# Performance work log

Hardware: AMD Instinct MI355X
Metric: run time of the kernel (lower is better)

Reference implementation:

```python
import jax, jax.numpy as jnp
import numpy as np

B, S, H, R = 32, 1024, 768, 24
ATT_EPS = 1e10
LN_EPS = 1e-12


def setup_inputs() -> dict:
    key = jax.random.key(0)
    ks = jax.random.split(key, 20)
    sc = 0.02
    inp = {
        "relation": jax.random.randint(ks[0], (B, 1), 0, R),
        "last_hidden_size": jax.random.normal(ks[1], (B, S, H), dtype=jnp.float32),
        "sub_head": jax.random.randint(ks[2], (B, 1), 0, S),
        "sub_tail": jax.random.randint(ks[3], (B, 1), 0, S),
        "attention_mask": jnp.ones((B, S), dtype=jnp.float32),
        # learned parameters
        "rel_emb": jax.random.normal(ks[4], (R, H)) * sc,
        "W_rf": jax.random.normal(ks[5], (H, H)) * sc,
        "b_rf": jnp.zeros((H,), jnp.float32),
        "gamma": jnp.ones((H,), jnp.float32),
        "beta": jnp.zeros((H,), jnp.float32),
        "W_wd": jax.random.normal(ks[6], (H, 2 * H)) * sc,
        "W_bd": jax.random.normal(ks[7], (H, 2 * H)) * sc,
        "Wq": jax.random.normal(ks[8], (H, H)) * sc,
        "bq": jnp.zeros((H,), jnp.float32),
        "Wk": jax.random.normal(ks[9], (H, H)) * sc,
        "bk": jnp.zeros((H,), jnp.float32),
        "Wv": jax.random.normal(ks[10], (H, H)) * sc,
        "bv": jnp.zeros((H,), jnp.float32),
        "W_obj": jax.random.normal(ks[11], (1, H)) * sc,
        "b_obj": jnp.zeros((1,), jnp.float32),
    }
    return inp


def reference(relation, last_hidden_size, sub_head, sub_tail, attention_mask,
              rel_emb, W_rf, b_rf, gamma, beta, W_wd, W_bd,
              Wq, bq, Wk, bk, Wv, bv, W_obj, b_obj):
    # dropout layers are identity in eval mode
    # relation feature: embedding -> linear -> ReLU6   [B,1,H]
    rel_feature = jnp.clip(rel_emb[relation] @ W_rf.T + b_rf, 0.0, 6.0)
    # subject span features via gather                 [B,1,H]
    sh = jnp.take_along_axis(last_hidden_size, sub_head[:, :, None], axis=1)
    st = jnp.take_along_axis(last_hidden_size, sub_tail[:, :, None], axis=1)
    sub_feature = (sh + st) * 0.5
    cond = jnp.concatenate([rel_feature, sub_feature], axis=-1)  # [B,1,2H]

    # conditional layer norm: per-sample affine from condition
    weight = cond @ W_wd.T + gamma  # [B,1,H]
    bias = cond @ W_bd.T + beta     # [B,1,H]
    mean = jnp.mean(last_hidden_size, axis=-1, keepdims=True)
    ctr = last_hidden_size - mean
    var = jnp.mean(ctr * ctr, axis=-1, keepdims=True)
    x = ctr / jnp.sqrt(var + LN_EPS)
    x = x * weight + bias  # [B,S,H]

    # custom attention: ReLU-activated q/k/v, additive mask bias, residual
    q = jax.nn.relu(x @ Wq.T + bq)
    k = jax.nn.relu(x @ Wk.T + bk)
    v = jax.nn.relu(x @ Wv.T + bv)
    e = jnp.einsum('bsh,bth->bst', q, k)  # [B,S,S]
    e = e - ATT_EPS * (1.0 - attention_mask[:, None, :])
    a = jax.nn.softmax(e, axis=-1)
    hidden = jnp.einsum('bst,bth->bsh', a, v) + x  # residual

    pred_obj_head = jnp.squeeze(hidden @ W_obj.T + b_obj, axis=-1)  # [B,S]
    return pred_obj_head, hidden
```

## Files before the change

kernel.cpp:

```cpp
#include <hip/hip_runtime.h>

constexpr int NB  = 32;
constexpr int NS  = 1024;
constexpr int NH  = 768;
constexpr int NH2 = 1536;
constexpr int NQKV = 2304;
constexpr int NBS = NB * NS;

typedef __bf16 bf16x8 __attribute__((ext_vector_type(8)));
typedef float  f32x4  __attribute__((ext_vector_type(4)));
typedef unsigned short u16x8 __attribute__((ext_vector_type(8)));

__device__ __forceinline__ unsigned short f2bf(float f) {
  unsigned int u = __builtin_bit_cast(unsigned int, f);
  u += 0x7FFFu + ((u >> 16) & 1u);
  return (unsigned short)(u >> 16);
}
__device__ __forceinline__ float bf2f(unsigned short h) {
  return __builtin_bit_cast(float, ((unsigned int)h) << 16);
}

#define GLDS16(g, l)                                                         \
  __builtin_amdgcn_global_load_lds(                                          \
      (__attribute__((address_space(1))) void*)(g),                          \
      (__attribute__((address_space(3))) void*)(l), 16, 0, 0)

__launch_bounds__(256)
__global__ void cond_pre(const int* __restrict__ relation,
                         const float* __restrict__ h,
                         const int* __restrict__ subh,
                         const int* __restrict__ subt,
                         const float* __restrict__ rel_emb,
                         float* __restrict__ reT, float* __restrict__ condT) {
  const int b = blockIdx.x, t = threadIdx.x;
  const int r = relation[b], sh = subh[b], st = subt[b];
  for (int k = t; k < NH; k += 256) {
    reT[(size_t)k * NB + b] = rel_emb[(size_t)r * NH + k];
    condT[(size_t)(NH + k) * NB + b] =
        0.5f * (h[((size_t)b * NS + sh) * NH + k] +
                h[((size_t)b * NS + st) * NH + k]);
  }
}

__launch_bounds__(256)
__global__ void cond_rf(const float* __restrict__ W_rf,
                        const float* __restrict__ b_rf,
                        const float* __restrict__ reT,
                        float* __restrict__ condT) {
  const int t = threadIdx.x;
  const int b = t & 31, jl = t >> 5;
  const int j = blockIdx.x * 8 + jl;
  const float4* w4 = (const float4*)(W_rf + (size_t)j * NH);
  const float* rT = reT + b;
  float a0 = 0.f, a1 = 0.f;
  for (int k4 = 0; k4 < NH / 4; k4++) {
    float4 w = w4[k4];
    const float* c = rT + (size_t)(k4 * 4) * NB;
    a0 += w.x * c[0] + w.y * c[NB];
    a1 += w.z * c[2 * NB] + w.w * c[3 * NB];
  }
  float acc = a0 + a1 + b_rf[j];
  condT[(size_t)j * NB + b] = fminf(fmaxf(acc, 0.0f), 6.0f);
}

__launch_bounds__(256)
__global__ void cond_wb(const float* __restrict__ W_wd,
                        const float* __restrict__ W_bd,
                        const float* __restrict__ gamma,
                        const float* __restrict__ beta,
                        const float* __restrict__ condT,
                        float* __restrict__ wt, float* __restrict__ bs) {
  __shared__ float redW[128], redB[128];
  const int t = threadIdx.x;
  const int b = t & 31, jl = (t >> 5) & 3, ks = t >> 7;
  const int j = blockIdx.x * 4 + jl;
  const float4* ww = (const float4*)(W_wd + (size_t)j * NH2 + ks * NH);
  const float4* wb = (const float4*)(W_bd + (size_t)j * NH2 + ks * NH);
  const float* cT = condT + (size_t)ks * NH * NB + b;
  float aw0 = 0.f, aw1 = 0.f, ab0 = 0.f, ab1 = 0.f;
  for (int k4 = 0; k4 < NH / 4; k4++) {
    float4 w = ww[k4];
    float4 v = wb[k4];
    const float* c = cT + (size_t)(k4 * 4) * NB;
    float c0 = c[0], c1 = c[NB], c2 = c[2 * NB], c3 = c[3 * NB];
    aw0 += w.x * c0 + w.y * c1;
    aw1 += w.z * c2 + w.w * c3;
    ab0 += v.x * c0 + v.y * c1;
    ab1 += v.z * c2 + v.w * c3;
  }
  float aw = aw0 + aw1, ab = ab0 + ab1;
  if (ks == 1) {
    redW[t - 128] = aw;
    redB[t - 128] = ab;
  }
  __syncthreads();
  if (ks == 0) {
    aw += redW[t];
    ab += redB[t];
    wt[(size_t)b * NH + j] = aw + gamma[j];
    bs[(size_t)b * NH + j] = ab + beta[j];
  }
}

__launch_bounds__(64)
__global__ void ln_kernel(const float* __restrict__ h,
                          const float* __restrict__ wt,
                          const float* __restrict__ bs,
                          unsigned short* __restrict__ xbf) {
  const int row = blockIdx.x;
  const int b = row >> 10;
  const int lane = threadIdx.x;
  const float4* hr = (const float4*)(h + (size_t)row * NH);
  float4 v0 = hr[lane], v1 = hr[lane + 64], v2 = hr[lane + 128];
  float sum = 0.f, sq = 0.f;
  {
    sum += v0.x + v0.y + v0.z + v0.w;
    sq  += v0.x * v0.x + v0.y * v0.y + v0.z * v0.z + v0.w * v0.w;
    sum += v1.x + v1.y + v1.z + v1.w;
    sq  += v1.x * v1.x + v1.y * v1.y + v1.z * v1.z + v1.w * v1.w;
    sum += v2.x + v2.y + v2.z + v2.w;
    sq  += v2.x * v2.x + v2.y * v2.y + v2.z * v2.z + v2.w * v2.w;
  }
  for (int off = 32; off > 0; off >>= 1) {
    sum += __shfl_xor(sum, off, 64);
    sq  += __shfl_xor(sq, off, 64);
  }
  const float mean = sum * (1.0f / NH);
  const float var  = sq * (1.0f / NH) - mean * mean;
  const float rstd = rsqrtf(var + 1e-12f);
  const float4* wr = (const float4*)(wt + (size_t)b * NH);
  const float4* br = (const float4*)(bs + (size_t)b * NH);
  ushort4* xr = (ushort4*)(xbf + (size_t)row * NH);
#pragma unroll
  for (int i = 0; i < 3; i++) {
    float4 v = (i == 0) ? v0 : (i == 1) ? v1 : v2;
    float4 w = wr[lane + 64 * i];
    float4 bb = br[lane + 64 * i];
    ushort4 o;
    o.x = f2bf((v.x - mean) * rstd * w.x + bb.x);
    o.y = f2bf((v.y - mean) * rstd * w.y + bb.y);
    o.z = f2bf((v.z - mean) * rstd * w.z + bb.z);
    o.w = f2bf((v.w - mean) * rstd * w.w + bb.w);
    xr[lane + 64 * i] = o;
  }
}

__launch_bounds__(256)
__global__ void prep_w(const float* __restrict__ Wq, const float* __restrict__ bq,
                       const float* __restrict__ Wk, const float* __restrict__ bk,
                       const float* __restrict__ Wv, const float* __restrict__ bv,
                       unsigned short* __restrict__ Wcat, float* __restrict__ bcat) {
  const int row = blockIdx.x;
  const float* Wsrc;
  const float* bsrc;
  int r;
  if (row < NH) { Wsrc = Wq; bsrc = bq; r = row; }
  else if (row < NH2) { Wsrc = Wk; bsrc = bk; r = row - NH; }
  else { Wsrc = Wv; bsrc = bv; r = row - NH2; }
  for (int j = threadIdx.x; j < NH; j += 256)
    Wcat[(size_t)row * NH + j] = f2bf(Wsrc[(size_t)r * NH + j]);
  if (threadIdx.x == 0) bcat[row] = bsrc[r];
}

template <int OUT_BF16, int RELU, int HASBIAS, int RES>
__launch_bounds__(256, 4)
__global__ void gemm128(const unsigned short* __restrict__ A, long long sAz, int lda,
                        const unsigned short* __restrict__ Bm, long long sBz, int ldb,
                        void* __restrict__ C, long long sCz, int ldc,
                        const float* __restrict__ bias,
                        const unsigned short* __restrict__ Res, long long sRz, int ldr,
                        int K) {
  __shared__ char lds[32768];
  const int t = threadIdx.x;
  const int gx = gridDim.x, gxy = gridDim.x * gridDim.y;
  int n = blockIdx.x + gridDim.x * (blockIdx.y + gridDim.y * blockIdx.z);
  int wid;
  {
    const int nwg = gxy * gridDim.z;
    const int q = nwg >> 3, r = nwg & 7;
    const int xcd = n & 7, lid = n >> 3;
    wid = (xcd < r ? xcd * (q + 1) : r * (q + 1) + (xcd - r) * q) + lid;
  }
  const int z = wid / gxy;
  const int rem = wid % gxy;
  const int tileN = (rem % gx) * 128;
  const int tileM = (rem / gx) * 128;
  const unsigned short* Ab = A + (size_t)z * sAz + (size_t)tileM * lda;
  const unsigned short* Bb = Bm + (size_t)z * sBz + (size_t)tileN * ldb;

  const int lane = t & 63;
  const int w = t >> 6;
  const int wm = w >> 1, wn = w & 1;
  const int lr = lane & 15, hi = lane >> 4;
  const int cbyte = ((hi ^ ((lr >> 1) & 3)) << 4);

  const int sgc = (t & 3) ^ ((t >> 3) & 3);

#define STAGEOP(Gb, ld, kc, dst)                                            \
  do {                                                                      \
    GLDS16((Gb) + (size_t)(t >> 2) * (ld) + (kc) + sgc * 8,                 \
           (dst) + (size_t)t * 16);                                         \
    GLDS16((Gb) + (size_t)(64 + (t >> 2)) * (ld) + (kc) + sgc * 8,          \
           (dst) + 4096 + (size_t)t * 16);                                  \
  } while (0)

  f32x4 acc[4][4];
#pragma unroll
  for (int m = 0; m < 4; m++)
#pragma unroll
    for (int n2 = 0; n2 < 4; n2++) acc[m][n2] = (f32x4)0.0f;

  const int NT = K >> 5;

  STAGEOP(Ab, lda, 0, lds);
  STAGEOP(Bb, ldb, 0, lds + 8192);
  __syncthreads();

  for (int kt = 0; kt < NT; kt++) {
    const int bb = kt & 1;
    const char* Ah = lds + bb * 16384;
    const char* Bh = Ah + 8192;
    if (kt + 1 < NT) {
      STAGEOP(Ab, lda, (kt + 1) * 32, lds + (bb ^ 1) * 16384);
      STAGEOP(Bb, ldb, (kt + 1) * 32, lds + (bb ^ 1) * 16384 + 8192);
    }
    bf16x8 aF[4], bF[4];
#pragma unroll
    for (int i = 0; i < 4; i++)
      aF[i] = *(const bf16x8*)(Ah + (wm * 64 + i * 16 + lr) * 64 + cbyte);
#pragma unroll
    for (int j = 0; j < 4; j++)
      bF[j] = *(const bf16x8*)(Bh + (wn * 64 + j * 16 + lr) * 64 + cbyte);
#pragma unroll
    for (int i = 0; i < 4; i++)
#pragma unroll
      for (int j = 0; j < 4; j++)
        acc[i][j] = __builtin_amdgcn_mfma_f32_16x16x32_bf16(aF[i], bF[j],
                                                            acc[i][j], 0, 0, 0);
    __syncthreads();
  }

  const int row0 = tileM + wm * 64;
  const int col0 = tileN + wn * 64;
#pragma unroll
  for (int m = 0; m < 4; m++) {
    const int rowb = row0 + m * 16 + hi * 4;
#pragma unroll
    for (int n2 = 0; n2 < 4; n2++) {
      const int col = col0 + n2 * 16 + lr;
      const float bv = HASBIAS ? bias[col] : 0.0f;
      f32x4 v = acc[m][n2];
#pragma unroll
      for (int r = 0; r < 4; r++) {
        float x = v[r] + bv;
        if (RELU) x = fmaxf(x, 0.0f);
        if (RES)
          x += bf2f(Res[(size_t)z * sRz + (size_t)(rowb + r) * ldr + col]);
        if (OUT_BF16)
          ((unsigned short*)C)[(size_t)z * sCz + (size_t)(rowb + r) * ldc + col] =
              f2bf(x);
        else
          ((float*)C)[(size_t)z * sCz + (size_t)(rowb + r) * ldc + col] = x;
      }
    }
  }
#undef STAGEOP
}

__launch_bounds__(256)
__global__ void softmax_kernel(float* __restrict__ e,
                               const float* __restrict__ mask, int b0) {
  const int ri = blockIdx.x;
  const int lb = blockIdx.y;
  const int b = b0 + lb;
  float* row = e + ((size_t)lb * NS + ri) * NS;
  const int t = threadIdx.x;
  float4 v = ((const float4*)row)[t];
  float4 m = ((const float4*)(mask + (size_t)b * NS))[t];
  v.x -= 1e10f * (1.0f - m.x);
  v.y -= 1e10f * (1.0f - m.y);
  v.z -= 1e10f * (1.0f - m.z);
  v.w -= 1e10f * (1.0f - m.w);
  float mx = fmaxf(fmaxf(v.x, v.y), fmaxf(v.z, v.w));
  __shared__ float red[4];
  for (int off = 32; off > 0; off >>= 1) mx = fmaxf(mx, __shfl_xor(mx, off, 64));
  if ((t & 63) == 0) red[t >> 6] = mx;
  __syncthreads();
  mx = fmaxf(fmaxf(red[0], red[1]), fmaxf(red[2], red[3]));
  const float e0 = __expf(v.x - mx), e1 = __expf(v.y - mx);
  const float e2 = __expf(v.z - mx), e3 = __expf(v.w - mx);
  float sm = e0 + e1 + e2 + e3;
  __syncthreads();
  for (int off = 32; off > 0; off >>= 1) sm += __shfl_xor(sm, off, 64);
  if ((t & 63) == 0) red[t >> 6] = sm;
  __syncthreads();
  sm = red[0] + red[1] + red[2] + red[3];
  const float inv = 1.0f / sm;
  ushort4 o;
  o.x = f2bf(e0 * inv);
  o.y = f2bf(e1 * inv);
  o.z = f2bf(e2 * inv);
  o.w = f2bf(e3 * inv);
  ((ushort4*)row)[t] = o;
}

__launch_bounds__(256)
__global__ void transpose_v(const unsigned short* __restrict__ qkv,
                            unsigned short* __restrict__ vT) {
  const int b = blockIdx.z;
  const int s0 = blockIdx.x * 64;
  const int h0 = blockIdx.y * 64;
  __shared__ unsigned short tile[64][72];
  const int t = threadIdx.x;
  const int tx = t & 7, ty = t >> 3;
  const unsigned short* src = qkv + ((size_t)(b * NS + s0)) * NQKV + NH2 + h0;
#pragma unroll
  for (int i = 0; i < 2; i++) {
    const int s = ty + 32 * i;
    u16x8 vv = *(const u16x8*)(src + (size_t)s * NQKV + tx * 8);
#pragma unroll
    for (int j = 0; j < 8; j++) tile[s][tx * 8 + j] = vv[j];
  }
  __syncthreads();
  unsigned short* dst = vT + ((size_t)b * NH + h0) * NS + s0;
#pragma unroll
  for (int i = 0; i < 2; i++) {
    const int hh = ty + 32 * i;
    u16x8 o;
#pragma unroll
    for (int j = 0; j < 8; j++) o[j] = tile[tx * 8 + j][hh];
    *(u16x8*)(dst + (size_t)hh * NS + tx * 8) = o;
  }
}

__launch_bounds__(64)
__global__ void pred_kernel(const float* __restrict__ hidden,
                            const float* __restrict__ wobj,
                            const float* __restrict__ bobj,
                            float* __restrict__ pred) {
  const int row = blockIdx.x;
  const int lane = threadIdx.x;
  const float4* hr = (const float4*)(hidden + (size_t)row * NH);
  const float4* wr = (const float4*)wobj;
  float s = 0.f;
#pragma unroll
  for (int i = 0; i < 3; i++) {
    float4 a = hr[lane + 64 * i];
    float4 w = wr[lane + 64 * i];
    s += a.x * w.x + a.y * w.y + a.z * w.z + a.w * w.w;
  }
  for (int off = 32; off > 0; off >>= 1) s += __shfl_xor(s, off, 64);
  if (lane == 0) pred[row] = s + bobj[0];
}

extern "C" void kernel_launch(void* const* d_in, const int* in_sizes, int n_in,
                              void* d_out, int out_size, void* d_ws,
                              size_t ws_size, hipStream_t stream) {
  const int* relation   = (const int*)d_in[0];
  const float* lhs      = (const float*)d_in[1];
  const int* sub_head   = (const int*)d_in[2];
  const int* sub_tail   = (const int*)d_in[3];
  const float* att_mask = (const float*)d_in[4];
  const float* rel_emb  = (const float*)d_in[5];
  const float* W_rf     = (const float*)d_in[6];
  const float* b_rf     = (const float*)d_in[7];
  const float* gamma    = (const float*)d_in[8];
  const float* beta     = (const float*)d_in[9];
  const float* W_wd     = (const float*)d_in[10];
  const float* W_bd     = (const float*)d_in[11];
  const float* Wq       = (const float*)d_in[12];
  const float* bq       = (const float*)d_in[13];
  const float* Wk       = (const float*)d_in[14];
  const float* bk       = (const float*)d_in[15];
  const float* Wv       = (const float*)d_in[16];
  const float* bv       = (const float*)d_in[17];
  const float* W_obj    = (const float*)d_in[18];
  const float* b_obj    = (const float*)d_in[19];

  char* ws = (char*)d_ws;
  unsigned short* Wcat = (unsigned short*)(ws + 0);
  float* bcat  = (float*)(ws + 3538944);
  float* wt    = (float*)(ws + 3548160);
  float* bs    = (float*)(ws + 3646464);
  float* reT   = (float*)(ws + 3744768);
  float* condT = (float*)(ws + 3843072);
  unsigned short* xbf = (unsigned short*)(ws + 4039680);
  unsigned short* qkv = (unsigned short*)(ws + 54371328);
  unsigned short* vT  = (unsigned short*)(ws + 205366272);
  float* ebuf = (float*)(ws + 255697920);

  float* out_pred = (float*)d_out;
  float* out_hidden = out_pred + NBS;

  const size_t fixed = 255697920ull;
  size_t avail = ws_size > fixed ? ws_size - fixed : 0;
  int CB = 32;
  while (CB > 1 && (size_t)CB * (size_t)NS * NS * 4 > avail) CB >>= 1;

  prep_w<<<dim3(NQKV), dim3(256), 0, stream>>>(Wq, bq, Wk, bk, Wv, bv, Wcat, bcat);
  cond_pre<<<dim3(NB), dim3(256), 0, stream>>>(relation, lhs, sub_head, sub_tail,
                                               rel_emb, reT, condT);
  cond_rf<<<dim3(NH / 8), dim3(256), 0, stream>>>(W_rf, b_rf, reT, condT);
  cond_wb<<<dim3(NH / 4), dim3(256), 0, stream>>>(W_wd, W_bd, gamma, beta, condT,
                                                  wt, bs);
  ln_kernel<<<dim3(NBS), dim3(64), 0, stream>>>(lhs, wt, bs, xbf);

  gemm128<1, 1, 1, 0><<<dim3(NQKV / 128, NBS / 128, 1), dim3(256), 0, stream>>>(
      xbf, 0, NH, Wcat, 0, NH, qkv, 0, NQKV, bcat, nullptr, 0, 0, NH);

  transpose_v<<<dim3(NS / 64, NH / 64, NB), dim3(256), 0, stream>>>(qkv, vT);

  for (int b0 = 0; b0 < NB; b0 += CB) {
    gemm128<0, 0, 0, 0><<<dim3(NS / 128, NS / 128, CB), dim3(256), 0, stream>>>(
        qkv + (size_t)b0 * NS * NQKV, (long long)NS * NQKV, NQKV,
        qkv + (size_t)b0 * NS * NQKV + NH, (long long)NS * NQKV, NQKV,
        ebuf, (long long)NS * NS, NS, nullptr, nullptr, 0, 0, NH);
    softmax_kernel<<<dim3(NS, CB), dim3(256), 0, stream>>>(ebuf, att_mask, b0);
    gemm128<0, 0, 0, 1><<<dim3(NH / 128, NS / 128, CB), dim3(256), 0, stream>>>(
        (const unsigned short*)ebuf, (long long)NS * 2048, 2048,
        vT + (size_t)b0 * NH * NS, (long long)NH * NS, NS,
        out_hidden + (size_t)b0 * NS * NH, (long long)NS * NH, NH, nullptr,
        xbf + (size_t)b0 * NS * NH, (long long)NS * NH, NH, NS);
  }

  pred_kernel<<<dim3(NBS), dim3(64), 0, stream>>>(out_hidden, W_obj, b_obj,
                                                  out_pred);
}
```

Measured before the change: 504.1 us.

## Split QKV into separate planes and write softmax probabilities to compact buffer

The QKV projection GEMM now writes Q, K and V into three separate contiguous [B*S, H] planes instead of one interleaved [B*S, 3H] buffer, so the QK^T GEMM and the V transpose read with a tighter stride. Softmax writes its bf16 probabilities into a separate dense buffer with row stride S rather than in place over the fp32 scores with a 2S stride. The PV GEMM then reads a compact A operand. This costs extra workspace per batch chunk, which may shrink the chunk size if workspace is tight.

```diff
diff --git a/kernel.cpp b/kernel.cpp
--- a/kernel.cpp
+++ b/kernel.cpp
@@ -162,7 +162,7 @@
   if (threadIdx.x == 0) bcat[row] = bsrc[r];
 }
 
-template <int OUT_BF16, int RELU, int HASBIAS, int RES>
+template <int OUT_BF16, int RELU, int HASBIAS, int RES, int SPLIT3>
 __launch_bounds__(256, 4)
 __global__ void gemm128(const unsigned short* __restrict__ A, long long sAz, int lda,
                         const unsigned short* __restrict__ Bm, long long sBz, int ldb,
@@ -250,17 +250,23 @@
       const int col = col0 + n2 * 16 + lr;
       const float bv = HASBIAS ? bias[col] : 0.0f;
       f32x4 v = acc[m][n2];
+      const int seg = SPLIT3 ? (col >= NH2 ? 2 : (col >= NH ? 1 : 0)) : 0;
+      const int csub = SPLIT3 ? col - seg * NH : col;
 #pragma unroll
       for (int r = 0; r < 4; r++) {
         float x = v[r] + bv;
         if (RELU) x = fmaxf(x, 0.0f);
         if (RES)
           x += bf2f(Res[(size_t)z * sRz + (size_t)(rowb + r) * ldr + col]);
-        if (OUT_BF16)
+        if (SPLIT3) {
+          ((unsigned short*)C)[(size_t)seg * NBS * NH +
+                               (size_t)(rowb + r) * NH + csub] = f2bf(x);
+        } else if (OUT_BF16) {
           ((unsigned short*)C)[(size_t)z * sCz + (size_t)(rowb + r) * ldc + col] =
               f2bf(x);
-        else
+        } else {
           ((float*)C)[(size_t)z * sCz + (size_t)(rowb + r) * ldc + col] = x;
+        }
       }
     }
   }
@@ -268,12 +274,13 @@
 }
 
 __launch_bounds__(256)
-__global__ void softmax_kernel(float* __restrict__ e,
+__global__ void softmax_kernel(const float* __restrict__ e,
+                               unsigned short* __restrict__ p,
                                const float* __restrict__ mask, int b0) {
   const int ri = blockIdx.x;
   const int lb = blockIdx.y;
   const int b = b0 + lb;
-  float* row = e + ((size_t)lb * NS + ri) * NS;
+  const float* row = e + ((size_t)lb * NS + ri) * NS;
   const int t = threadIdx.x;
   float4 v = ((const float4*)row)[t];
   float4 m = ((const float4*)(mask + (size_t)b * NS))[t];
@@ -301,11 +308,11 @@
   o.y = f2bf(e1 * inv);
   o.z = f2bf(e2 * inv);
   o.w = f2bf(e3 * inv);
-  ((ushort4*)row)[t] = o;
-}
-
-__launch_bounds__(256)
-__global__ void transpose_v(const unsigned short* __restrict__ qkv,
+  ((ushort4*)(p + ((size_t)lb * NS + ri) * NS))[t] = o;
+}
+
+__launch_bounds__(256)
+__global__ void transpose_v(const unsigned short* __restrict__ vc,
                             unsigned short* __restrict__ vT) {
   const int b = blockIdx.z;
   const int s0 = blockIdx.x * 64;
@@ -313,11 +320,11 @@
   __shared__ unsigned short tile[64][72];
   const int t = threadIdx.x;
   const int tx = t & 7, ty = t >> 3;
-  const unsigned short* src = qkv + ((size_t)(b * NS + s0)) * NQKV + NH2 + h0;
+  const unsigned short* src = vc + ((size_t)(b * NS + s0)) * NH + h0;
 #pragma unroll
   for (int i = 0; i < 2; i++) {
     const int s = ty + 32 * i;
-    u16x8 vv = *(const u16x8*)(src + (size_t)s * NQKV + tx * 8);
+    u16x8 vv = *(const u16x8*)(src + (size_t)s * NH + tx * 8);
 #pragma unroll
     for (int j = 0; j < 8; j++) tile[s][tx * 8 + j] = vv[j];
   }
@@ -387,7 +394,7 @@
   unsigned short* xbf = (unsigned short*)(ws + 4039680);
   unsigned short* qkv = (unsigned short*)(ws + 54371328);
   unsigned short* vT  = (unsigned short*)(ws + 205366272);
-  float* ebuf = (float*)(ws + 255697920);
+  char* attbuf = ws + 255697920;
 
   float* out_pred = (float*)d_out;
   float* out_hidden = out_pred + NBS;
@@ -395,7 +402,11 @@
   const size_t fixed = 255697920ull;
   size_t avail = ws_size > fixed ? ws_size - fixed : 0;
   int CB = 32;
-  while (CB > 1 && (size_t)CB * (size_t)NS * NS * 4 > avail) CB >>= 1;
+  while (CB > 1 && (size_t)CB * ((size_t)NS * NS * 4 + (size_t)NS * NS * 2) > avail)
+    CB >>= 1;
+  float* ebuf = (float*)attbuf;
+  unsigned short* pbuf =
+      (unsigned short*)(attbuf + (size_t)CB * NS * NS * 4);
 
   prep_w<<<dim3(NQKV), dim3(256), 0, stream>>>(Wq, bq, Wk, bk, Wv, bv, Wcat, bcat);
   cond_pre<<<dim3(NB), dim3(256), 0, stream>>>(relation, lhs, sub_head, sub_tail,
@@ -405,19 +416,21 @@
                                                   wt, bs);
   ln_kernel<<<dim3(NBS), dim3(64), 0, stream>>>(lhs, wt, bs, xbf);
 
-  gemm128<1, 1, 1, 0><<<dim3(NQKV / 128, NBS / 128, 1), dim3(256), 0, stream>>>(
-      xbf, 0, NH, Wcat, 0, NH, qkv, 0, NQKV, bcat, nullptr, 0, 0, NH);
-
-  transpose_v<<<dim3(NS / 64, NH / 64, NB), dim3(256), 0, stream>>>(qkv, vT);
+  gemm128<1, 1, 1, 0, 1><<<dim3(NQKV / 128, NBS / 128, 1), dim3(256), 0, stream>>>(
+      xbf, 0, NH, Wcat, 0, NH, qkv, 0, NH, bcat, nullptr, 0, 0, NH);
+
+  transpose_v<<<dim3(NS / 64, NH / 64, NB), dim3(256), 0, stream>>>(
+      qkv + (size_t)2 * NBS * NH, vT);
 
   for (int b0 = 0; b0 < NB; b0 += CB) {
-    gemm128<0, 0, 0, 0><<<dim3(NS / 128, NS / 128, CB), dim3(256), 0, stream>>>(
-        qkv + (size_t)b0 * NS * NQKV, (long long)NS * NQKV, NQKV,
-        qkv + (size_t)b0 * NS * NQKV + NH, (long long)NS * NQKV, NQKV,
+    gemm128<0, 0, 0, 0, 0><<<dim3(NS / 128, NS / 128, CB), dim3(256), 0, stream>>>(
+        qkv + (size_t)b0 * NS * NH, (long long)NS * NH, NH,
+        qkv + (size_t)NBS * NH + (size_t)b0 * NS * NH, (long long)NS * NH, NH,
         ebuf, (long long)NS * NS, NS, nullptr, nullptr, 0, 0, NH);
-    softmax_kernel<<<dim3(NS, CB), dim3(256), 0, stream>>>(ebuf, att_mask, b0);
-    gemm128<0, 0, 0, 1><<<dim3(NH / 128, NS / 128, CB), dim3(256), 0, stream>>>(
-        (const unsigned short*)ebuf, (long long)NS * 2048, 2048,
+    softmax_kernel<<<dim3(NS, CB), dim3(256), 0, stream>>>(ebuf, pbuf, att_mask,
+                                                           b0);
+    gemm128<0, 0, 0, 1, 0><<<dim3(NH / 128, NS / 128, CB), dim3(256), 0, stream>>>(
+        pbuf, (long long)NS * NS, NS,
         vT + (size_t)b0 * NH * NS, (long long)NH * NS, NS,
         out_hidden + (size_t)b0 * NS * NH, (long long)NS * NH, NH, nullptr,
         xbf + (size_t)b0 * NS * NH, (long long)NS * NH, NH, NS);
```

After: 515.1 us. 1.02x slower.
